# Kernel optimization log

Measured on AMD Instinct MI355X. Metric: run time of the kernel, lower is better.

The kernel has to match this reference:

```python
import jax, jax.numpy as jnp
import numpy as np

B, S, HID = 2, 2048, 1024
NH, HD = 4, 256
SCALE = HD ** -0.5


def _rope(x, fr, fi):
    # x: [B,S,NH,HD]; fr/fi: [S,HD//2]
    b, s, n, d = x.shape
    xr = x.reshape(b, s, n, d // 2, 2)
    re, im = xr[..., 0], xr[..., 1]
    fr = fr[None, :, None, :]
    fi = fi[None, :, None, :]
    rr = re * fr - im * fi
    ri = re * fi + im * fr
    return jnp.stack((rr, ri), axis=-1).reshape(b, s, n, d)


def setup_inputs() -> dict:
    key = jax.random.key(0)
    k1, k2, k3 = jax.random.split(key, 3)
    hidden_states = jax.random.normal(k1, (B, S, HID), dtype=jnp.float32)
    # RoPE frequencies (standard theta=10000)
    inv_freq = 1.0 / (10000.0 ** (np.arange(0, HD, 2, dtype=np.float32) / HD))  # [HD//2]
    t = np.arange(S, dtype=np.float32)
    ang = np.outer(t, inv_freq)  # [S, HD//2]
    freqs_real = jnp.asarray(np.cos(ang), dtype=jnp.float32)
    freqs_imag = jnp.asarray(np.sin(ang), dtype=jnp.float32)
    # causal additive mask [1,1,S,S]
    causal = jnp.tril(jnp.ones((S, S), dtype=bool))
    mask = jnp.where(causal, 0.0, -1e9).astype(jnp.float32)[None, None]
    W_qkv = jax.random.normal(k2, (3 * HID, HID), dtype=jnp.float32) * (HID ** -0.5)
    W_o = jax.random.normal(k3, (HID, HID), dtype=jnp.float32) * (HID ** -0.5)
    return {"hidden_states": hidden_states, "freqs_real": freqs_real,
            "freqs_imag": freqs_imag, "mask": mask, "W_qkv": W_qkv, "W_o": W_o}


def reference(hidden_states, freqs_real, freqs_imag, mask, W_qkv, W_o):
    b, s, _ = hidden_states.shape
    qkv = hidden_states @ W_qkv.T  # [B,S,3*HID]
    qkv = qkv.reshape(b, s, 3, NH, HD)
    q, k, v = qkv[:, :, 0], qkv[:, :, 1], qkv[:, :, 2]
    q = _rope(q, freqs_real, freqs_imag)
    k = _rope(k, freqs_real, freqs_imag)
    scores = jnp.einsum('bqhd,bkhd->bhqk', q * SCALE, k) + mask  # [B,NH,S,S]
    probs = jax.nn.softmax(scores, axis=-1)
    attn = jnp.einsum('bhqk,bkhd->bqhd', probs, v).reshape(b, s, HID)
    return attn @ W_o.T
```

## Files before the change

kernel.cpp:

```cpp
#include <hip/hip_runtime.h>
#include <stdint.h>

#define NB 2
#define NS 2048
#define NHID 1024
#define NHEADS 4
#define DHEAD 256
#define NP 128
#define QK_SCALE 0.0625f

typedef unsigned short ushort_t;
typedef __bf16 bf16x8 __attribute__((ext_vector_type(8)));
typedef float floatx4 __attribute__((ext_vector_type(4)));
typedef short shortx8 __attribute__((ext_vector_type(8)));
typedef unsigned short ushortx4 __attribute__((ext_vector_type(4)));
typedef unsigned short ushortx8 __attribute__((ext_vector_type(8)));

__device__ __forceinline__ float bf2f(ushort_t u) {
    unsigned int x = ((unsigned int)u) << 16;
    return __builtin_bit_cast(float, x);
}
__device__ __forceinline__ ushort_t f2bf(float f) {
    unsigned int u = __builtin_bit_cast(unsigned int, f);
    u += 0x7fff + ((u >> 16) & 1);
    return (ushort_t)(u >> 16);
}

__device__ __forceinline__ floatx4 mfma16(bf16x8 a, bf16x8 b, floatx4 c) {
    return __builtin_amdgcn_mfma_f32_16x16x32_bf16(a, b, c, 0, 0, 0);
}

__device__ __forceinline__ void gload_lds16(const void* g, void* l) {
    __builtin_amdgcn_global_load_lds(
        (const __attribute__((address_space(1))) void*)g,
        (__attribute__((address_space(3))) void*)l, 16, 0, 0);
}

#define N4_H (4096 * 1024 / 4)
#define N4_WQ (3072 * 1024 / 4)
#define N4_WO (1024 * 1024 / 4)
__global__ __launch_bounds__(256) void cast3_kernel(const float* __restrict__ inH,
                                                    const float* __restrict__ inWq,
                                                    const float* __restrict__ inWo,
                                                    ushort_t* __restrict__ out) {
    int i = blockIdx.x * 256 + threadIdx.x;
    const float* src;
    int j = i;
    if (i < N4_H) {
        src = inH;
    } else if (i < N4_H + N4_WQ) {
        src = inWq; j = i - N4_H;
    } else {
        src = inWo; j = i - (N4_H + N4_WQ);
    }
    float4 v = ((const float4*)src)[j];
    ushortx4 o = { f2bf(v.x), f2bf(v.y), f2bf(v.z), f2bf(v.w) };
    ((ushortx4*)out)[i] = o;
}


__global__ __launch_bounds__(256) void gemm_bt_f32s(const ushort_t* __restrict__ A,
                                                    const ushort_t* __restrict__ Bt,
                                                    float* __restrict__ C0,
                                                    float* __restrict__ C1,
                                                    int M, int N, int K) {
    __shared__ ushort_t sA[128 * 64];
    __shared__ ushort_t sB[128 * 64];
    const int t = threadIdx.x;
    const int m0 = blockIdx.y * 128;
    const int n0 = blockIdx.x * 128;
    const int kz = blockIdx.z;
    float* Cout = kz ? C1 : C0;
    const int kbeg = kz * (K / 2), kend = kbeg + K / 2;
    const int w = t >> 6, l = t & 63;
    const int wm = (w >> 1) * 64, wn = (w & 1) * 64;
    const int lc = l & 15, lq = l >> 4;

    floatx4 acc[4][4];
#pragma unroll
    for (int i = 0; i < 4; i++)
#pragma unroll
        for (int j = 0; j < 4; j++) acc[i][j] = (floatx4){0.f, 0.f, 0.f, 0.f};

    const int srow = w * 8 + (l >> 3);
    const int scol = ((((l & 7) - (l >> 3)) & 7)) * 8;
    const ushort_t* Ag = A + (size_t)(m0 + srow) * K + scol;
    const ushort_t* Bg = Bt + (size_t)(n0 + srow) * K + scol;
    ushort_t* lA = &sA[(size_t)t * 8];
    ushort_t* lB = &sB[(size_t)t * 8];

    for (int kk = kbeg; kk < kend; kk += 64) {
        __syncthreads();
#pragma unroll
        for (int j = 0; j < 4; j++) {
            gload_lds16(Ag + kk + (size_t)j * 32 * K, lA + j * 2048);
            gload_lds16(Bg + kk + (size_t)j * 32 * K, lB + j * 2048);
        }
        __syncthreads();
#pragma unroll
        for (int ks = 0; ks < 2; ks++) {
            bf16x8 af[4], bfv[4];
#pragma unroll
            for (int i = 0; i < 4; i++) {
                int R = wm + i * 16 + lc;
                af[i] = *(const bf16x8*)&sA[R * 64 + ((ks * 4 + lq + R) & 7) * 8];
            }
#pragma unroll
            for (int j = 0; j < 4; j++) {
                int R = wn + j * 16 + lc;
                bfv[j] = *(const bf16x8*)&sB[R * 64 + ((ks * 4 + lq + R) & 7) * 8];
            }
#pragma unroll
            for (int i = 0; i < 4; i++)
#pragma unroll
                for (int j = 0; j < 4; j++)
                    acc[i][j] = mfma16(af[i], bfv[j], acc[i][j]);
        }
    }

#pragma unroll
    for (int i = 0; i < 4; i++) {
        int row = m0 + wm + i * 16 + lq * 4;
#pragma unroll
        for (int j = 0; j < 4; j++) {
            int col = n0 + wn + j * 16 + lc;
#pragma unroll
            for (int r = 0; r < 4; r++)
                Cout[(size_t)(row + r) * N + col] = acc[i][j][r];
        }
    }
}

__global__ __launch_bounds__(256) void add_f32(const float* __restrict__ a,
                                               const float* __restrict__ b,
                                               float* __restrict__ o, int n4) {
    int i = blockIdx.x * 256 + threadIdx.x;
    if (i < n4) {
        float4 x = ((const float4*)a)[i];
        float4 y = ((const float4*)b)[i];
        float4 z = { x.x + y.x, x.y + y.y, x.z + y.z, x.w + y.w };
        ((float4*)o)[i] = z;
    }
}

__global__ __launch_bounds__(256) void gemm_qkv(const ushort_t* __restrict__ A,
                                                const ushort_t* __restrict__ Bt,
                                                const float* __restrict__ fre,
                                                const float* __restrict__ fim,
                                                ushort_t* __restrict__ Q,
                                                ushort_t* __restrict__ Kk,
                                                ushort_t* __restrict__ Vt) {
    const int M_K = 1024;
    __shared__ ushort_t sA[128 * 64];
    __shared__ ushort_t sB[128 * 64];
    const int t = threadIdx.x;
    const int m0 = blockIdx.y * 128;
    const int n0 = blockIdx.x * 128;
    const int w = t >> 6, l = t & 63;
    const int wm = (w >> 1) * 64, wn = (w & 1) * 64;
    const int lc = l & 15, lq = l >> 4;

    floatx4 acc[4][4];
#pragma unroll
    for (int i = 0; i < 4; i++)
#pragma unroll
        for (int j = 0; j < 4; j++) acc[i][j] = (floatx4){0.f, 0.f, 0.f, 0.f};

    const int srow = w * 8 + (l >> 3);
    const int scol = ((((l & 7) - (l >> 3)) & 7)) * 8;
    const ushort_t* Ag = A + (size_t)(m0 + srow) * M_K + scol;
    const ushort_t* Bg = Bt + (size_t)(n0 + srow) * M_K + scol;
    ushort_t* lA = &sA[(size_t)t * 8];
    ushort_t* lB = &sB[(size_t)t * 8];

    for (int kk = 0; kk < M_K; kk += 64) {
        __syncthreads();
#pragma unroll
        for (int j = 0; j < 4; j++) {
            gload_lds16(Ag + kk + (size_t)j * 32 * M_K, lA + j * 2048);
            gload_lds16(Bg + kk + (size_t)j * 32 * M_K, lB + j * 2048);
        }
        __syncthreads();
#pragma unroll
        for (int ks = 0; ks < 2; ks++) {
            bf16x8 af[4], bfv[4];
#pragma unroll
            for (int i = 0; i < 4; i++) {
                int R = wm + i * 16 + lc;
                af[i] = *(const bf16x8*)&sA[R * 64 + ((ks * 4 + lq + R) & 7) * 8];
            }
#pragma unroll
            for (int j = 0; j < 4; j++) {
                int R = wn + j * 16 + lc;
                bfv[j] = *(const bf16x8*)&sB[R * 64 + ((ks * 4 + lq + R) & 7) * 8];
            }
#pragma unroll
            for (int i = 0; i < 4; i++)
#pragma unroll
                for (int j = 0; j < 4; j++)
                    acc[i][j] = mfma16(af[i], bfv[j], acc[i][j]);
        }
    }

    const int sect = n0 >> 10;
#pragma unroll
    for (int i = 0; i < 4; i++) {
        int row = m0 + wm + i * 16 + lq * 4;
        int b = row >> 11;
        int srow2 = row & 2047;
#pragma unroll
        for (int j = 0; j < 4; j++) {
            int col = n0 + wn + j * 16 + lc;
            int d = col & 255;
            int h = (col >> 8) & 3;
            int bh = b * NHEADS + h;
            if (sect == 2) {
                ushortx4 pack = { f2bf(acc[i][j][0]), f2bf(acc[i][j][1]),
                                  f2bf(acc[i][j][2]), f2bf(acc[i][j][3]) };
                *(ushortx4*)&Vt[((size_t)bh * 256 + d) * NS + srow2] = pack;
            } else {
                int p = d >> 1;
                int odd = d & 1;
                ushort_t* dst = (sect == 0) ? Q : Kk;
#pragma unroll
                for (int r = 0; r < 4; r++) {
                    float v = acc[i][j][r];
                    float vp = __shfl_xor(v, 1);
                    int s = srow2 + r;
                    float c = fre[s * NP + p], si = fim[s * NP + p];
                    float out = odd ? (vp * si + v * c) : (v * c - vp * si);
                    if (sect == 0) out *= QK_SCALE;
                    dst[((size_t)bh * NS + s) * DHEAD + d] = f2bf(out);
                }
            }
        }
    }
}

#define BQ3 128
#define BKV3 64
#define PPAD 72
#define CHCAP 6
#define NPART_BH 51
#define OPART_SPLIT 224

__global__ __launch_bounds__(256, 2) void flash_attn4(const ushort_t* __restrict__ Q,
                                                      const ushort_t* __restrict__ K,
                                                      const ushort_t* __restrict__ Vt,
                                                      ushort_t* __restrict__ OpA,
                                                      ushort_t* __restrict__ OpB,
                                                      float* __restrict__ ml) {
    __shared__ ushort_t sK[BKV3 * 256];
    __shared__ ushort_t sV[DHEAD * 64];
    __shared__ ushort_t sP[4][16 * PPAD];

    int rem = blockIdx.x, qt = 15, nsp;
    for (;;) {
        nsp = (2 * (qt + 1) + CHCAP - 1) / CHCAP;
        if (rem < nsp) break;
        rem -= nsp;
        qt--;
    }
    const int nch = 2 * (qt + 1);
    const int cbeg = rem * CHCAP;
    const int cend = (cbeg + CHCAP < nch) ? cbeg + CHCAP : nch;

    const int h = blockIdx.y, b = blockIdx.z;
    const int t = threadIdx.x, w = t >> 6, l = t & 63;
    const int lc = l & 15, lq = l >> 4;
    const int bh = b * NHEADS + h;
    const size_t base = (size_t)bh * NS * DHEAD;
    const int q0 = qt * BQ3;

    const int krb = w * 2 + (l >> 5);
    const int kck = ((l & 31) - (krb & 7)) & 31;
    const size_t koff = (size_t)krb * 256 + kck * 8;
    const int vrb = w * 8 + (l >> 3);
    const int vck = ((l & 7) - (vrb & 7)) & 7;
    const size_t voff = (size_t)vrb * NS + vck * 8;
    ushort_t* dK = &sK[w * 512 + l * 8];
    ushort_t* dV = &sV[w * 512 + l * 8];

    bf16x8 qf[2][8];
#pragma unroll
    for (int gq = 0; gq < 2; gq++) {
        const ushort_t* qrow = Q + base + (size_t)(q0 + w * 32 + gq * 16 + lc) * DHEAD + lq * 8;
#pragma unroll
        for (int dk = 0; dk < 8; dk++) qf[gq][dk] = *(const bf16x8*)(qrow + dk * 32);
    }

    floatx4 accO[2][16];
#pragma unroll
    for (int gq = 0; gq < 2; gq++)
#pragma unroll
        for (int j = 0; j < 16; j++) accO[gq][j] = (floatx4){0.f, 0.f, 0.f, 0.f};
    float lrun[2][4] = {{0.f, 0.f, 0.f, 0.f}, {0.f, 0.f, 0.f, 0.f}};

    for (int kc = cbeg; kc < cend; kc++) {
        const int kb = kc * BKV3;
        __syncthreads();
        {
            const ushort_t* ksrc = K + base + (size_t)kb * 256 + koff;
            const ushort_t* vsrc = Vt + base + kb + voff;
#pragma unroll
            for (int j = 0; j < 8; j++)
                gload_lds16(ksrc + j * (8 * 256), dK + j * 2048);
#pragma unroll
            for (int j = 0; j < 8; j++)
                gload_lds16(vsrc + j * (32 * NS), dV + j * 2048);
        }
        __syncthreads();

        floatx4 sfr[2][4];
#pragma unroll
        for (int gq = 0; gq < 2; gq++)
#pragma unroll
            for (int g = 0; g < 4; g++) sfr[gq][g] = (floatx4){0.f, 0.f, 0.f, 0.f};
#pragma unroll
        for (int dk = 0; dk < 8; dk++) {
#pragma unroll
            for (int g = 0; g < 4; g++) {
                int R = g * 16 + lc;
                int phys = (dk * 4 + lq + (R & 7)) & 31;
                bf16x8 bk = *(const bf16x8*)&sK[R * 256 + phys * 8];
                sfr[0][g] = mfma16(qf[0][dk], bk, sfr[0][g]);
                sfr[1][g] = mfma16(qf[1][dk], bk, sfr[1][g]);
            }
        }

        if (kc >= nch - 2) {
#pragma unroll
            for (int gq = 0; gq < 2; gq++)
#pragma unroll
                for (int g = 0; g < 4; g++) {
                    int kg = kb + g * 16 + lc;
                    int qr = q0 + w * 32 + gq * 16 + lq * 4;
#pragma unroll
                    for (int r = 0; r < 4; r++)
                        if (kg > qr + r) sfr[gq][g][r] = -1e30f;
                }
        }

        ushort_t* pw = sP[w];
#pragma unroll
        for (int gq = 0; gq < 2; gq++) {
#pragma unroll
            for (int g = 0; g < 4; g++)
#pragma unroll
                for (int r = 0; r < 4; r++) {
                    float p = __expf(sfr[gq][g][r]);
                    lrun[gq][r] += p;
                    pw[(lq * 4 + r) * PPAD + g * 16 + lc] = f2bf(p);
                }
            bf16x8 ap0 = *(const bf16x8*)&pw[lc * PPAD + lq * 8];
            bf16x8 ap1 = *(const bf16x8*)&pw[lc * PPAD + 32 + lq * 8];
#pragma unroll
            for (int j = 0; j < 16; j++) {
                int D = j * 16 + lc;
                int ph0 = (lq + (D & 7)) & 7;
                int ph1 = (4 + lq + (D & 7)) & 7;
                bf16x8 bv0 = *(const bf16x8*)&sV[D * 64 + ph0 * 8];
                bf16x8 bv1 = *(const bf16x8*)&sV[D * 64 + ph1 * 8];
                accO[gq][j] = mfma16(ap0, bv0, accO[gq][j]);
                accO[gq][j] = mfma16(ap1, bv1, accO[gq][j]);
            }
        }
    }

    const int pid = bh * NPART_BH + blockIdx.x;
    ushort_t* op = (pid < OPART_SPLIT) ? OpA + (size_t)pid * (128 * 256)
                                       : OpB + (size_t)(pid - OPART_SPLIT) * (128 * 256);
#pragma unroll
    for (int gq = 0; gq < 2; gq++) {
#pragma unroll
        for (int r = 0; r < 4; r++) {
            int row = w * 32 + gq * 16 + lq * 4 + r;
#pragma unroll
            for (int j = 0; j < 16; j++)
                op[row * 256 + j * 16 + lc] = f2bf(accO[gq][j][r]);
            float lv = lrun[gq][r];
#pragma unroll
            for (int off = 1; off < 16; off <<= 1) lv += __shfl_xor(lv, off);
            if (lc == 0) ml[(size_t)pid * 128 + row] = lv;
        }
    }
}

__global__ __launch_bounds__(256) void combine_parts2(const ushort_t* __restrict__ OpA,
                                                      const ushort_t* __restrict__ OpB,
                                                      const float* __restrict__ ml,
                                                      ushort_t* __restrict__ O) {
    const int qt = blockIdx.x >> 3, rsub = blockIdx.x & 7;
    const int h = blockIdx.y, b = blockIdx.z;
    const int bh = b * NHEADS + h;
    int bbase = 0;
    for (int q = 15; q > qt; q--) bbase += (2 * (q + 1) + CHCAP - 1) / CHCAP;
    const int nsp = (2 * (qt + 1) + CHCAP - 1) / CHCAP;
    const int pid0 = bh * NPART_BH + bbase;

    const int t = threadIdx.x;
    const int rl = t >> 4;
    const int c0 = (t & 15) * 16;
    const int row = rsub * 16 + rl;

    float so[16];
#pragma unroll
    for (int k = 0; k < 16; k++) so[k] = 0.f;
    float sl = 0.f;

    for (int i = 0; i < nsp; i++) {
        int pid = pid0 + i;
        const ushort_t* op = (pid < OPART_SPLIT)
                                 ? OpA + (size_t)pid * (128 * 256)
                                 : OpB + (size_t)(pid - OPART_SPLIT) * (128 * 256);
        const ushort_t* p = op + row * 256 + c0;
        ushortx8 a0 = *(const ushortx8*)p;
        ushortx8 a1 = *(const ushortx8*)(p + 8);
#pragma unroll
        for (int k = 0; k < 8; k++) {
            so[k] += bf2f(a0[k]);
            so[8 + k] += bf2f(a1[k]);
        }
        sl += ml[(size_t)pid * 128 + row];
    }

    float inv = 1.f / sl;
    ushortx8 o0, o1;
#pragma unroll
    for (int k = 0; k < 8; k++) {
        o0[k] = f2bf(so[k] * inv);
        o1[k] = f2bf(so[8 + k] * inv);
    }
    int s = qt * BQ3 + row;
    ushort_t* dst = O + ((size_t)(b * NS + s) * NHEADS + h) * DHEAD + c0;
    *(ushortx8*)dst = o0;
    *(ushortx8*)(dst + 8) = o1;
}

extern "C" void kernel_launch(void* const* d_in, const int* in_sizes, int n_in,
                              void* d_out, int out_size, void* d_ws, size_t ws_size,
                              hipStream_t stream) {
    const float* hidden = (const float*)d_in[0];
    const float* fre = (const float*)d_in[1];
    const float* fim = (const float*)d_in[2];
    const float* Wqkv = (const float*)d_in[4];
    const float* Wo = (const float*)d_in[5];

    char* ws = (char*)d_ws;
    ushort_t* hb    = (ushort_t*)(ws);
    ushort_t* wqkvb = (ushort_t*)(ws + 8388608);
    ushort_t* wob   = (ushort_t*)(ws + 14680064);
    ushort_t* qb    = (ushort_t*)(ws + 16777216);
    ushort_t* kb    = (ushort_t*)(ws + 25165824);
    ushort_t* vtb   = (ushort_t*)(ws + 33554432);
    ushort_t* OpA   = (ushort_t*)(ws);
    ushort_t* OpB   = (ushort_t*)(ws + 41943040);
    ushort_t* oattn = (ushort_t*)(ws + 16777216);
    float*    gP0   = (float*)(ws + 25165824);
    float*    gP1   = (float*)(ws + 41943040);
    float*    ml    = (float*)(ws + 58720256);

    cast3_kernel<<<(N4_H + N4_WQ + N4_WO) / 256, 256, 0, stream>>>(hidden, Wqkv, Wo, hb);

    gemm_qkv<<<dim3(3072 / 128, 4096 / 128), 256, 0, stream>>>(
        hb, wqkvb, fre, fim, qb, kb, vtb);

    flash_attn4<<<dim3(NPART_BH, NHEADS, NB), 256, 0, stream>>>(qb, kb, vtb, OpA, OpB, ml);
    combine_parts2<<<dim3(128, NHEADS, NB), 256, 0, stream>>>(OpA, OpB, ml, oattn);

    gemm_bt_f32s<<<dim3(1024 / 128, 4096 / 128, 2), 256, 0, stream>>>(
        oattn, wob, gP0, gP1, 4096, 1024, 1024);
    add_f32<<<4096, 256, 0, stream>>>(gP0, gP1, (float*)d_out, 4096 * 1024 / 4);
}
```

Measured before the change: 210.9 us.

## Double-buffer LDS tiles in QKV and output GEMMs to overlap loads with MFMA

Both bf16 GEMM kernels now use two LDS buffers per operand. The next K-tile's global-to-LDS loads are issued before computing on the current tile, and one barrier per stage replaces the two per iteration. The goal is to hide global load latency behind MFMA work. LDS use doubles to 64KB per block, which may lower occupancy. The loop also assumes an even number of stages.

Result: no change. 211.7 us (+0.4%).

```diff
diff --git a/kernel.cpp b/kernel.cpp
--- a/kernel.cpp
+++ b/kernel.cpp
@@ -64,14 +64,17 @@
                                                     float* __restrict__ C0,
                                                     float* __restrict__ C1,
                                                     int M, int N, int K) {
-    __shared__ ushort_t sA[128 * 64];
-    __shared__ ushort_t sB[128 * 64];
+    __shared__ ushort_t sA0[128 * 64];
+    __shared__ ushort_t sA1[128 * 64];
+    __shared__ ushort_t sB0[128 * 64];
+    __shared__ ushort_t sB1[128 * 64];
     const int t = threadIdx.x;
     const int m0 = blockIdx.y * 128;
     const int n0 = blockIdx.x * 128;
     const int kz = blockIdx.z;
     float* Cout = kz ? C1 : C0;
-    const int kbeg = kz * (K / 2), kend = kbeg + K / 2;
+    const int kbeg = kz * (K / 2);
+    const int nst = (K / 2) / 64;
     const int w = t >> 6, l = t & 63;
     const int wm = (w >> 1) * 64, wn = (w & 1) * 64;
     const int lc = l & 15, lq = l >> 4;
@@ -84,31 +87,30 @@
 
     const int srow = w * 8 + (l >> 3);
     const int scol = ((((l & 7) - (l >> 3)) & 7)) * 8;
-    const ushort_t* Ag = A + (size_t)(m0 + srow) * K + scol;
-    const ushort_t* Bg = Bt + (size_t)(n0 + srow) * K + scol;
-    ushort_t* lA = &sA[(size_t)t * 8];
-    ushort_t* lB = &sB[(size_t)t * 8];
-
-    for (int kk = kbeg; kk < kend; kk += 64) {
-        __syncthreads();
+    const ushort_t* Ag = A + (size_t)(m0 + srow) * K + scol + kbeg;
+    const ushort_t* Bg = Bt + (size_t)(n0 + srow) * K + scol + kbeg;
+    const int lofs = t * 8;
+
+    auto stage = [&](ushort_t* lA, ushort_t* lB, int kk) {
 #pragma unroll
         for (int j = 0; j < 4; j++) {
             gload_lds16(Ag + kk + (size_t)j * 32 * K, lA + j * 2048);
             gload_lds16(Bg + kk + (size_t)j * 32 * K, lB + j * 2048);
         }
-        __syncthreads();
+    };
+    auto compute = [&](const ushort_t* cA, const ushort_t* cB) {
 #pragma unroll
         for (int ks = 0; ks < 2; ks++) {
             bf16x8 af[4], bfv[4];
 #pragma unroll
             for (int i = 0; i < 4; i++) {
                 int R = wm + i * 16 + lc;
-                af[i] = *(const bf16x8*)&sA[R * 64 + ((ks * 4 + lq + R) & 7) * 8];
+                af[i] = *(const bf16x8*)&cA[R * 64 + ((ks * 4 + lq + R) & 7) * 8];
             }
 #pragma unroll
             for (int j = 0; j < 4; j++) {
                 int R = wn + j * 16 + lc;
-                bfv[j] = *(const bf16x8*)&sB[R * 64 + ((ks * 4 + lq + R) & 7) * 8];
+                bfv[j] = *(const bf16x8*)&cB[R * 64 + ((ks * 4 + lq + R) & 7) * 8];
             }
 #pragma unroll
             for (int i = 0; i < 4; i++)
@@ -116,6 +118,22 @@
                 for (int j = 0; j < 4; j++)
                     acc[i][j] = mfma16(af[i], bfv[j], acc[i][j]);
         }
+    };
+
+    stage(&sA0[lofs], &sB0[lofs], 0);
+    asm volatile("s_waitcnt vmcnt(0)" ::: "memory");
+    __builtin_amdgcn_s_barrier();
+
+#pragma unroll 1
+    for (int s = 0; s < nst; s += 2) {
+        if (s + 1 < nst) stage(&sA1[lofs], &sB1[lofs], (s + 1) * 64);
+        compute(sA0, sB0);
+        asm volatile("s_waitcnt vmcnt(0)" ::: "memory");
+        __builtin_amdgcn_s_barrier();
+        if (s + 2 < nst) stage(&sA0[lofs], &sB0[lofs], (s + 2) * 64);
+        compute(sA1, sB1);
+        asm volatile("s_waitcnt vmcnt(0)" ::: "memory");
+        __builtin_amdgcn_s_barrier();
     }
 
 #pragma unroll
@@ -151,8 +169,10 @@
                                                 ushort_t* __restrict__ Kk,
                                                 ushort_t* __restrict__ Vt) {
     const int M_K = 1024;
-    __shared__ ushort_t sA[128 * 64];
-    __shared__ ushort_t sB[128 * 64];
+    __shared__ ushort_t sA0[128 * 64];
+    __shared__ ushort_t sA1[128 * 64];
+    __shared__ ushort_t sB0[128 * 64];
+    __shared__ ushort_t sB1[128 * 64];
     const int t = threadIdx.x;
     const int m0 = blockIdx.y * 128;
     const int n0 = blockIdx.x * 128;
@@ -170,29 +190,28 @@
     const int scol = ((((l & 7) - (l >> 3)) & 7)) * 8;
     const ushort_t* Ag = A + (size_t)(m0 + srow) * M_K + scol;
     const ushort_t* Bg = Bt + (size_t)(n0 + srow) * M_K + scol;
-    ushort_t* lA = &sA[(size_t)t * 8];
-    ushort_t* lB = &sB[(size_t)t * 8];
-
-    for (int kk = 0; kk < M_K; kk += 64) {
-        __syncthreads();
+    const int lofs = t * 8;
+
+    auto stage = [&](ushort_t* lA, ushort_t* lB, int kk) {
 #pragma unroll
         for (int j = 0; j < 4; j++) {
             gload_lds16(Ag + kk + (size_t)j * 32 * M_K, lA + j * 2048);
             gload_lds16(Bg + kk + (size_t)j * 32 * M_K, lB + j * 2048);
         }
-        __syncthreads();
+    };
+    auto compute = [&](const ushort_t* cA, const ushort_t* cB) {
 #pragma unroll
         for (int ks = 0; ks < 2; ks++) {
             bf16x8 af[4], bfv[4];
 #pragma unroll
             for (int i = 0; i < 4; i++) {
                 int R = wm + i * 16 + lc;
-                af[i] = *(const bf16x8*)&sA[R * 64 + ((ks * 4 + lq + R) & 7) * 8];
+                af[i] = *(const bf16x8*)&cA[R * 64 + ((ks * 4 + lq + R) & 7) * 8];
             }
 #pragma unroll
             for (int j = 0; j < 4; j++) {
                 int R = wn + j * 16 + lc;
-                bfv[j] = *(const bf16x8*)&sB[R * 64 + ((ks * 4 + lq + R) & 7) * 8];
+                bfv[j] = *(const bf16x8*)&cB[R * 64 + ((ks * 4 + lq + R) & 7) * 8];
             }
 #pragma unroll
             for (int i = 0; i < 4; i++)
@@ -200,6 +219,22 @@
                 for (int j = 0; j < 4; j++)
                     acc[i][j] = mfma16(af[i], bfv[j], acc[i][j]);
         }
+    };
+
+    stage(&sA0[lofs], &sB0[lofs], 0);
+    asm volatile("s_waitcnt vmcnt(0)" ::: "memory");
+    __builtin_amdgcn_s_barrier();
+
+#pragma unroll 1
+    for (int s = 0; s < 16; s += 2) {
+        if (s + 1 < 16) stage(&sA1[lofs], &sB1[lofs], (s + 1) * 64);
+        compute(sA0, sB0);
+        asm volatile("s_waitcnt vmcnt(0)" ::: "memory");
+        __builtin_amdgcn_s_barrier();
+        if (s + 2 < 16) stage(&sA0[lofs], &sB0[lofs], (s + 2) * 64);
+        compute(sA1, sB1);
+        asm volatile("s_waitcnt vmcnt(0)" ::: "memory");
+        __builtin_amdgcn_s_barrier();
     }
 
     const int sect = n0 >> 10;
```

## Double-buffer QKV GEMM LDS loads and remap blocks for XCD-local L2 reuse

Applied to the files above, without the earlier changes.

The QKV projection GEMM now uses two LDS buffers, so the global-to-LDS load of the next K-slice is issued while MFMAs run on the current one, with one barrier per stage instead of two. Both GEMMs switch to a flattened 1D grid whose block index is decoded so that blocks landing on the same XCD (round-robin by blockIdx mod 8) share M/N tiles, aiming for better L2 reuse. The cost is double the LDS per block for the QKV GEMM, which may lower occupancy, and the decoding hardcodes the grid shape.

New measurement: 212.2 us. No clear change (+0.7%).

```diff
diff --git a/kernel.cpp b/kernel.cpp
--- a/kernel.cpp
+++ b/kernel.cpp
@@ -67,9 +67,14 @@
     __shared__ ushort_t sA[128 * 64];
     __shared__ ushort_t sB[128 * 64];
     const int t = threadIdx.x;
-    const int m0 = blockIdx.y * 128;
-    const int n0 = blockIdx.x * 128;
-    const int kz = blockIdx.z;
+    const int f = blockIdx.x;
+    const int xcd = f & 7;
+    const int idx = f >> 3;
+    const int im = idx >> 4;
+    const int in = (idx >> 1) & 7;
+    const int kz = idx & 1;
+    const int m0 = (xcd * 4 + im) * 128;
+    const int n0 = in * 128;
     float* Cout = kz ? C1 : C0;
     const int kbeg = kz * (K / 2), kend = kbeg + K / 2;
     const int w = t >> 6, l = t & 63;
@@ -151,11 +156,18 @@
                                                 ushort_t* __restrict__ Kk,
                                                 ushort_t* __restrict__ Vt) {
     const int M_K = 1024;
-    __shared__ ushort_t sA[128 * 64];
-    __shared__ ushort_t sB[128 * 64];
+    __shared__ ushort_t sA0[128 * 64];
+    __shared__ ushort_t sA1[128 * 64];
+    __shared__ ushort_t sB0[128 * 64];
+    __shared__ ushort_t sB1[128 * 64];
     const int t = threadIdx.x;
-    const int m0 = blockIdx.y * 128;
-    const int n0 = blockIdx.x * 128;
+    const int f = blockIdx.x;
+    const int xcd = f & 7;
+    const int idx = f >> 3;
+    const int mr = xcd & 3, nr = xcd >> 2;
+    const int im = idx & 7, in = idx >> 3;
+    const int m0 = (mr * 8 + im) * 128;
+    const int n0 = (nr * 12 + in) * 128;
     const int w = t >> 6, l = t & 63;
     const int wm = (w >> 1) * 64, wn = (w & 1) * 64;
     const int lc = l & 15, lq = l >> 4;
@@ -170,29 +182,28 @@
     const int scol = ((((l & 7) - (l >> 3)) & 7)) * 8;
     const ushort_t* Ag = A + (size_t)(m0 + srow) * M_K + scol;
     const ushort_t* Bg = Bt + (size_t)(n0 + srow) * M_K + scol;
-    ushort_t* lA = &sA[(size_t)t * 8];
-    ushort_t* lB = &sB[(size_t)t * 8];
-
-    for (int kk = 0; kk < M_K; kk += 64) {
-        __syncthreads();
+    const int lofs = t * 8;
+
+    auto stage = [&](ushort_t* lA, ushort_t* lB, int kk) {
 #pragma unroll
         for (int j = 0; j < 4; j++) {
             gload_lds16(Ag + kk + (size_t)j * 32 * M_K, lA + j * 2048);
             gload_lds16(Bg + kk + (size_t)j * 32 * M_K, lB + j * 2048);
         }
-        __syncthreads();
+    };
+    auto compute = [&](const ushort_t* cA, const ushort_t* cB) {
 #pragma unroll
         for (int ks = 0; ks < 2; ks++) {
             bf16x8 af[4], bfv[4];
 #pragma unroll
             for (int i = 0; i < 4; i++) {
                 int R = wm + i * 16 + lc;
-                af[i] = *(const bf16x8*)&sA[R * 64 + ((ks * 4 + lq + R) & 7) * 8];
+                af[i] = *(const bf16x8*)&cA[R * 64 + ((ks * 4 + lq + R) & 7) * 8];
             }
 #pragma unroll
             for (int j = 0; j < 4; j++) {
                 int R = wn + j * 16 + lc;
-                bfv[j] = *(const bf16x8*)&sB[R * 64 + ((ks * 4 + lq + R) & 7) * 8];
+                bfv[j] = *(const bf16x8*)&cB[R * 64 + ((ks * 4 + lq + R) & 7) * 8];
             }
 #pragma unroll
             for (int i = 0; i < 4; i++)
@@ -200,6 +211,22 @@
                 for (int j = 0; j < 4; j++)
                     acc[i][j] = mfma16(af[i], bfv[j], acc[i][j]);
         }
+    };
+
+    stage(&sA0[lofs], &sB0[lofs], 0);
+    asm volatile("s_waitcnt vmcnt(0)" ::: "memory");
+    __builtin_amdgcn_s_barrier();
+
+#pragma unroll 1
+    for (int s = 0; s < 16; s += 2) {
+        if (s + 1 < 16) stage(&sA1[lofs], &sB1[lofs], (s + 1) * 64);
+        compute(sA0, sB0);
+        asm volatile("s_waitcnt vmcnt(0)" ::: "memory");
+        __builtin_amdgcn_s_barrier();
+        if (s + 2 < 16) stage(&sA0[lofs], &sB0[lofs], (s + 2) * 64);
+        compute(sA1, sB1);
+        asm volatile("s_waitcnt vmcnt(0)" ::: "memory");
+        __builtin_amdgcn_s_barrier();
     }
 
     const int sect = n0 >> 10;
@@ -462,13 +489,13 @@
 
     cast3_kernel<<<(N4_H + N4_WQ + N4_WO) / 256, 256, 0, stream>>>(hidden, Wqkv, Wo, hb);
 
-    gemm_qkv<<<dim3(3072 / 128, 4096 / 128), 256, 0, stream>>>(
+    gemm_qkv<<<dim3(768), 256, 0, stream>>>(
         hb, wqkvb, fre, fim, qb, kb, vtb);
 
     flash_attn4<<<dim3(NPART_BH, NHEADS, NB), 256, 0, stream>>>(qb, kb, vtb, OpA, OpB, ml);
     combine_parts2<<<dim3(128, NHEADS, NB), 256, 0, stream>>>(OpA, OpB, ml, oattn);
 
-    gemm_bt_f32s<<<dim3(1024 / 128, 4096 / 128, 2), 256, 0, stream>>>(
+    gemm_bt_f32s<<<dim3(512), 256, 0, stream>>>(
         oattn, wob, gP0, gP1, 4096, 1024, 1024);
     add_f32<<<4096, 256, 0, stream>>>(gP0, gP1, (float*)d_out, 4096 * 1024 / 4);
 }
```
